# Performance work log

Hardware: AMD Instinct MI355X
Metric: run time of the kernel (lower is better)

## Reference

```python
import math
import jax, jax.numpy as jnp
import numpy as np

N_HEAD = 16
D_MODEL = 1024
D_K = 64
D_V = 64


def setup_inputs() -> dict:
    key = jax.random.key(0)
    ks = jax.random.split(key, 9)
    bs, s = 8, 1024
    q = jax.random.normal(ks[0], (bs, s, D_K), dtype=jnp.float32)
    k = jax.random.normal(ks[1], (bs, s, D_K), dtype=jnp.float32)
    v = jax.random.normal(ks[2], (bs, s, D_V), dtype=jnp.float32)
    # NOTE: the source module only ever uses linear_q (applied to q, k, v alike),
    # so we only materialize that projection. Torch Linear: y = x @ W.T + b.
    Wq = jax.random.normal(ks[3], (N_HEAD * D_K, D_K), dtype=jnp.float32) * 0.02
    bq = jnp.zeros((N_HEAD * D_K,), dtype=jnp.float32)
    W1 = jax.random.normal(ks[4], (D_MODEL, N_HEAD * D_V), dtype=jnp.float32) * 0.02
    b1 = jnp.zeros((D_MODEL,), dtype=jnp.float32)
    W2 = jax.random.normal(ks[5], (D_MODEL, D_MODEL), dtype=jnp.float32) * 0.02
    b2 = jnp.zeros((D_MODEL,), dtype=jnp.float32)
    return {"q": q, "k": k, "v": v, "Wq": Wq, "bq": bq,
            "W1": W1, "b1": b1, "W2": W2, "b2": b2}


def reference(q, k, v, Wq, bq, W1, b1, W2, b2):
    bs, s_q, d_k = q.shape
    h = N_HEAD
    scale = math.sqrt(d_k)
    # shared projection (source uses linear_q for all three); split heads on last dim
    proj = lambda x: (jnp.einsum('bsd,ed->bse', x, Wq) + bq).reshape(bs, -1, h, d_k)
    qh = proj(q)   # [b, s_q, h, d]
    kh = proj(k)   # [b, s_k, h, d]
    vh = proj(v)   # [b, s_v, h, d]
    e = jnp.einsum('bqhd,bkhd->bhqk', qh, kh) / scale
    a = jax.nn.softmax(e, axis=-1)  # dropout = identity in eval mode
    y = jnp.einsum('bhqk,bkhd->bqhd', a, vh).reshape(bs, s_q, h * d_k)
    # output MLP: Linear -> ReLU -> (dropout) -> Linear
    x = jax.nn.relu(jnp.einsum('bsd,ed->bse', y, W1) + b1)
    x = jnp.einsum('bsd,ed->bse', x, W2) + b2
    return x
```

## Files before the change

kernel.cpp:

```cpp
#include <hip/hip_runtime.h>
#include <math.h>

#define NB 8
#define SS 1024
#define NH 16
#define DK 64
#define EE 1024
#define DMOD 1024

using bf16x8 = __attribute__((ext_vector_type(8))) short;
using f32x4  = __attribute__((ext_vector_type(4))) float;

__device__ __forceinline__ unsigned short f2bf(float f) {
    unsigned u = __builtin_bit_cast(unsigned, f);
    u += 0x7FFFu + ((u >> 16) & 1u);
    return (unsigned short)(u >> 16);
}

__device__ __forceinline__ float exp2_hw(float x) {
#if __has_builtin(__builtin_amdgcn_exp2f)
    return __builtin_amdgcn_exp2f(x);
#else
    float r; asm("v_exp_f32 %0, %1" : "=v"(r) : "v"(x)); return r;
#endif
}

__device__ __forceinline__ unsigned cvt_pk_bf16(float lo, float hi) {
    unsigned r;
    asm("v_cvt_pk_bf16_f32 %0, %1, %2" : "=v"(r) : "v"(lo), "v"(hi));
    return r;
}

__device__ __forceinline__ void gld16(const void* g, void* l) {
    __builtin_amdgcn_global_load_lds(
        (const __attribute__((address_space(1))) void*)g,
        (__attribute__((address_space(3))) void*)l, 16, 0, 0);
}

__global__ __launch_bounds__(256) void cvt_all(
    const float* __restrict__ W1, const float* __restrict__ W2,
    const float* __restrict__ q, const float* __restrict__ k,
    const float* __restrict__ v, const float* __restrict__ Wq,
    unsigned short* __restrict__ W1b, unsigned short* __restrict__ W2b,
    unsigned short* __restrict__ qb, unsigned short* __restrict__ kb,
    unsigned short* __restrict__ vb, unsigned short* __restrict__ Wqb)
{
    const int z = blockIdx.y;
    const float* s; unsigned short* d; int n;
    switch (z) {
        case 0:  s = W1; d = W1b; n = 1048576; break;
        case 1:  s = W2; d = W2b; n = 1048576; break;
        case 2:  s = q;  d = qb;  n = 524288;  break;
        case 3:  s = k;  d = kb;  n = 524288;  break;
        case 4:  s = v;  d = vb;  n = 524288;  break;
        default: s = Wq; d = Wqb; n = 65536;   break;
    }
    const int i = (blockIdx.x * 256 + threadIdx.x) * 8;
    if (i >= n) return;
    const float4 a = *(const float4*)(s + i);
    const float4 b = *(const float4*)(s + i + 4);
    bf16x8 o;
    o[0]=(short)f2bf(a.x); o[1]=(short)f2bf(a.y); o[2]=(short)f2bf(a.z); o[3]=(short)f2bf(a.w);
    o[4]=(short)f2bf(b.x); o[5]=(short)f2bf(b.y); o[6]=(short)f2bf(b.z); o[7]=(short)f2bf(b.w);
    *(bf16x8*)(d + i) = o;
}

__global__ __launch_bounds__(256) void proj_mfma(
    const unsigned short* __restrict__ qb, const unsigned short* __restrict__ kb,
    const unsigned short* __restrict__ vb, const unsigned short* __restrict__ Wb,
    const float* __restrict__ bias, unsigned short* __restrict__ Cbase,
    float qscale)
{
    __shared__ __align__(16) unsigned short As[128 * 64];
    __shared__ __align__(16) unsigned short Bs[128 * 64];
    const int z = blockIdx.z;
    const unsigned short* X = (z == 0) ? qb : (z == 1) ? kb : vb;
    unsigned short* C = Cbase + (size_t)z * 8388608;
    const float sc = (z == 0) ? qscale : 1.0f;
    const int tid  = threadIdx.x;
    const int lane = tid & 63;
    const int w = tid >> 6, wm = w >> 1, wn = w & 1;
    const int n0 = blockIdx.x * 128, m0 = blockIdx.y * 128;
    const int lr = lane & 15, lg = lane >> 4;

    #pragma unroll
    for (int p = 0; p < 4; ++p) {
        const int c = p * 256 + tid;
        const int lb = (p * 256 + (tid & ~63)) * 8;
        gld16(X  + (size_t)m0 * DK + (size_t)c * 8, As + lb);
        gld16(Wb + (size_t)n0 * DK + (size_t)c * 8, Bs + lb);
    }
    __syncthreads();

    f32x4 acc[4][4] = {};
    #pragma unroll
    for (int kk = 0; kk < 2; ++kk) {
        bf16x8 af[4], bfr[4];
        #pragma unroll
        for (int mf = 0; mf < 4; ++mf)
            af[mf] = *(const bf16x8*)&As[(wm * 64 + mf * 16 + lr) * 64 + kk * 32 + lg * 8];
        #pragma unroll
        for (int nf = 0; nf < 4; ++nf)
            bfr[nf] = *(const bf16x8*)&Bs[(wn * 64 + nf * 16 + lr) * 64 + kk * 32 + lg * 8];
        #pragma unroll
        for (int mf = 0; mf < 4; ++mf)
            #pragma unroll
            for (int nf = 0; nf < 4; ++nf)
                acc[mf][nf] = __builtin_amdgcn_mfma_f32_16x16x32_bf16(
                    af[mf], bfr[nf], acc[mf][nf], 0, 0, 0);
    }

    #pragma unroll
    for (int nf = 0; nf < 4; ++nf) {
        const int n = n0 + wn * 64 + nf * 16 + lr;
        const float bb = bias[n];
        #pragma unroll
        for (int mf = 0; mf < 4; ++mf)
            #pragma unroll
            for (int r = 0; r < 4; ++r) {
                const int mr = m0 + wm * 64 + mf * 16 + lg * 4 + r;
                const int bh = (mr >> 10) * NH + (n >> 6);
                const int s  = mr & 1023, d = n & 63;
                const size_t idx = (z == 2)
                    ? (size_t)bh * 65536 + (size_t)d * 1024 + s
                    : (size_t)bh * 65536 + (size_t)s * 64 + d;
                C[idx] = f2bf((acc[mf][nf][r] + bb) * sc);
            }
    }
}

__global__ __launch_bounds__(256) void attn_v13(
    const unsigned short* __restrict__ Qp, const unsigned short* __restrict__ Kp,
    const unsigned short* __restrict__ Vt, unsigned short* __restrict__ Y)
{
    __shared__ __align__(16) unsigned short Ks[64 * 64];
    __shared__ __align__(16) unsigned short Vs[64 * 64];
    __shared__ __align__(16) unsigned short Ps[4][32][72];
    const int tid  = threadIdx.x;
    const int lane = tid & 63;
    const int w    = tid >> 6;
    const int flat    = blockIdx.x;
    const int logical = (flat & 7) * 128 + (flat >> 3);
    const int qt = logical & 7;
    const int bh = logical >> 3;
    const int q0 = qt * 128;
    const size_t base = (size_t)bh * (SS * DK);
    const int lr = lane & 15, lg = lane >> 4;
    const int lg4 = lg * 4;

    const int c0 = tid,       r0 = c0 >> 3, h0 = c0 & 7;
    const int c1 = 256 + tid, r1 = c1 >> 3, h1 = c1 & 7;
    const int lds0 = r0 * 64 + ((h0 ^ (r0 & 7)) << 3);
    const int lds1 = r1 * 64 + ((h1 ^ (r1 & 7)) << 3);

    const unsigned short* kbase = Kp + base;
    const unsigned short* vbase = Vt + base;
    bf16x8 kA = *(const bf16x8*)(kbase + (size_t)r0 * DK + h0 * 8);
    bf16x8 kB = *(const bf16x8*)(kbase + (size_t)r1 * DK + h1 * 8);
    bf16x8 vA = *(const bf16x8*)(vbase + (size_t)r0 * SS + h0 * 8);
    bf16x8 vB = *(const bf16x8*)(vbase + (size_t)r1 * SS + h1 * 8);
    *(bf16x8*)&Ks[lds0] = kA; *(bf16x8*)&Ks[lds1] = kB;
    *(bf16x8*)&Vs[lds0] = vA; *(bf16x8*)&Vs[lds1] = vB;

    bf16x8 bQ[2][2];
    #pragma unroll
    for (int qf = 0; qf < 2; ++qf) {
        const unsigned short* qptr =
            Qp + base + (size_t)(q0 + w * 32 + qf * 16 + lr) * DK + lg * 8;
        bQ[qf][0] = *(const bf16x8*)qptr;
        bQ[qf][1] = *(const bf16x8*)(qptr + 32);
    }

    __syncthreads();

    float lacc[2] = {0.0f, 0.0f};
    f32x4 oacc[2][4] = {};

    for (int kt = 0; kt < 16; ++kt) {
        if (kt < 15) {
            const int s1 = (kt + 1) * 64;
            kA = *(const bf16x8*)(kbase + (size_t)(s1 + r0) * DK + h0 * 8);
            kB = *(const bf16x8*)(kbase + (size_t)(s1 + r1) * DK + h1 * 8);
            vA = *(const bf16x8*)(vbase + (size_t)r0 * SS + s1 + h0 * 8);
            vB = *(const bf16x8*)(vbase + (size_t)r1 * SS + s1 + h1 * 8);
        }

        f32x4 sacc[2][4];
        #pragma unroll
        for (int nb = 0; nb < 4; ++nb) {
            const int krow = nb * 16 + lr;
            const bf16x8 aK0 = *(const bf16x8*)&Ks[krow * 64 + ((lg       ^ (lr & 7)) << 3)];
            const bf16x8 aK1 = *(const bf16x8*)&Ks[krow * 64 + (((4 + lg) ^ (lr & 7)) << 3)];
            #pragma unroll
            for (int qf = 0; qf < 2; ++qf) {
                f32x4 z = {};
                z = __builtin_amdgcn_mfma_f32_16x16x32_bf16(aK0, bQ[qf][0], z, 0, 0, 0);
                z = __builtin_amdgcn_mfma_f32_16x16x32_bf16(aK1, bQ[qf][1], z, 0, 0, 0);
                sacc[qf][nb] = z;
            }
        }

        bf16x8 bV[2][4];
        #pragma unroll
        for (int kk = 0; kk < 2; ++kk)
            #pragma unroll
            for (int d0 = 0; d0 < 4; ++d0) {
                const int vrow = d0 * 16 + lr;
                bV[kk][d0] = *(const bf16x8*)&Vs[vrow * 64 + (((kk * 4 + lg) ^ (lr & 7)) << 3)];
            }

        #pragma unroll
        for (int qf = 0; qf < 2; ++qf) {
            float p[4][4];
            float ls0 = 0.0f, ls1 = 0.0f;
            #pragma unroll
            for (int nb = 0; nb < 4; ++nb) {
                #pragma unroll
                for (int r = 0; r < 4; ++r) {
                    const float pv = exp2_hw(sacc[qf][nb][r]);
                    p[nb][r] = pv;
                    if (r & 1) ls1 += pv; else ls0 += pv;
                }
            }
            lacc[qf] += ls0 + ls1;

            #pragma unroll
            for (int nb = 0; nb < 4; ++nb) {
                uint2 pw;
                pw.x = cvt_pk_bf16(p[nb][0], p[nb][1]);
                pw.y = cvt_pk_bf16(p[nb][2], p[nb][3]);
                *(uint2*)&Ps[w][qf * 16 + lr][nb * 16 + lg4] = pw;
            }

            #pragma unroll
            for (int kk = 0; kk < 2; ++kk) {
                const bf16x8 aP = *(const bf16x8*)&Ps[w][qf * 16 + lr][kk * 32 + lg * 8];
                #pragma unroll
                for (int d0 = 0; d0 < 4; ++d0)
                    oacc[qf][d0] = __builtin_amdgcn_mfma_f32_16x16x32_bf16(
                        aP, bV[kk][d0], oacc[qf][d0], 0, 0, 0);
            }
        }

        if (kt < 15) {
            __syncthreads();
            *(bf16x8*)&Ks[lds0] = kA; *(bf16x8*)&Ks[lds1] = kB;
            *(bf16x8*)&Vs[lds0] = vA; *(bf16x8*)&Vs[lds1] = vB;
            __syncthreads();
        }
    }

    const int hh = bh & 15, bb = bh >> 4;
    #pragma unroll
    for (int qf = 0; qf < 2; ++qf) {
        float l = lacc[qf];
        l += __shfl_xor(l, 16);
        l += __shfl_xor(l, 32);
        const float linv = 1.0f / l;
        #pragma unroll
        for (int r = 0; r < 4; ++r) {
            const float lri = __shfl(linv, lg4 + r, 16);
            const int qr = q0 + w * 32 + qf * 16 + lg4 + r;
            unsigned short* dst = Y + (size_t)(bb * SS + qr) * EE + hh * DK;
            #pragma unroll
            for (int d0 = 0; d0 < 4; ++d0)
                dst[d0 * 16 + lr] = f2bf(oacc[qf][d0][r] * lri);
        }
    }
}

template<bool RELU, bool OUT_BF16>
__global__ __launch_bounds__(256) void mlp_gemm(
    const unsigned short* __restrict__ A, const unsigned short* __restrict__ B,
    const float* __restrict__ bias, void* __restrict__ Cv)
{
    constexpr int K = 1024, N = 1024;
    __shared__ __align__(16) unsigned short As[2][128 * 64];
    __shared__ __align__(16) unsigned short Bs[2][128 * 64];
    const int tid  = threadIdx.x;
    const int lane = tid & 63;
    const int w = tid >> 6, wm = w >> 1, wn = w & 1;
    const int flat    = blockIdx.x;
    const int logical = (flat & 7) * 64 + (flat >> 3);
    const int n0 = (logical & 7) * 128, m0 = (logical >> 3) * 128;
    const int lr = lane & 15, lg = lane >> 4;

    #pragma unroll
    for (int p = 0; p < 4; ++p) {
        const int c = p * 256 + tid;
        const int row = c >> 3, col = (c & 7) * 8;
        const int lb = (p * 256 + (tid & ~63)) * 8;
        gld16(A + (size_t)(m0 + row) * K + col, As[0] + lb);
        gld16(B + (size_t)(n0 + row) * K + col, Bs[0] + lb);
    }
    __syncthreads();

    f32x4 acc[4][4] = {};

    #pragma unroll
    for (int kt = 0; kt < 16; ++kt) {
        const int cur = kt & 1;
        if (kt < 15) {
            const int ko = (kt + 1) * 64;
            #pragma unroll
            for (int p = 0; p < 4; ++p) {
                const int c = p * 256 + tid;
                const int row = c >> 3, col = (c & 7) * 8;
                const int lb = (p * 256 + (tid & ~63)) * 8;
                gld16(A + (size_t)(m0 + row) * K + ko + col, As[cur ^ 1] + lb);
                gld16(B + (size_t)(n0 + row) * K + ko + col, Bs[cur ^ 1] + lb);
            }
        }
        #pragma unroll
        for (int kk = 0; kk < 2; ++kk) {
            bf16x8 af[4], bfr[4];
            #pragma unroll
            for (int mf = 0; mf < 4; ++mf)
                af[mf] = *(const bf16x8*)&As[cur][(wm * 64 + mf * 16 + lr) * 64 + kk * 32 + lg * 8];
            #pragma unroll
            for (int nf = 0; nf < 4; ++nf)
                bfr[nf] = *(const bf16x8*)&Bs[cur][(wn * 64 + nf * 16 + lr) * 64 + kk * 32 + lg * 8];
            #pragma unroll
            for (int mf = 0; mf < 4; ++mf)
                #pragma unroll
                for (int nf = 0; nf < 4; ++nf)
                    acc[mf][nf] = __builtin_amdgcn_mfma_f32_16x16x32_bf16(
                        af[mf], bfr[nf], acc[mf][nf], 0, 0, 0);
        }
        __syncthreads();
    }

    #pragma unroll
    for (int nf = 0; nf < 4; ++nf) {
        const int cc = n0 + wn * 64 + nf * 16 + lr;
        const float bb = bias[cc];
        #pragma unroll
        for (int mf = 0; mf < 4; ++mf) {
            #pragma unroll
            for (int r = 0; r < 4; ++r) {
                float x = acc[mf][nf][r] + bb;
                if (RELU) x = fmaxf(x, 0.0f);
                const size_t rr = (size_t)(m0 + wm * 64 + mf * 16 + lg * 4 + r);
                if (OUT_BF16) ((unsigned short*)Cv)[rr * N + cc] = f2bf(x);
                else          ((float*)Cv)[rr * N + cc] = x;
            }
        }
    }
}

extern "C" void kernel_launch(void* const* d_in, const int* in_sizes, int n_in,
                              void* d_out, int out_size, void* d_ws, size_t ws_size,
                              hipStream_t stream) {
    const float* q  = (const float*)d_in[0];
    const float* k  = (const float*)d_in[1];
    const float* v  = (const float*)d_in[2];
    const float* Wq = (const float*)d_in[3];
    const float* bq = (const float*)d_in[4];
    const float* W1 = (const float*)d_in[5];
    const float* b1 = (const float*)d_in[6];
    const float* W2 = (const float*)d_in[7];
    const float* b2 = (const float*)d_in[8];

    unsigned short* wsu = (unsigned short*)d_ws;
    unsigned short* Qp  = wsu;
    unsigned short* Kp  = wsu + (size_t)8388608;
    unsigned short* Vt  = wsu + (size_t)16777216;
    unsigned short* Y   = wsu + (size_t)25165824;
    unsigned short* W1b = wsu + (size_t)33554432;
    unsigned short* W2b = wsu + (size_t)34603008;
    unsigned short* qb  = wsu + (size_t)35651584;
    unsigned short* kb  = wsu + (size_t)36175872;
    unsigned short* vb  = wsu + (size_t)36700160;
    unsigned short* Wqb = wsu + (size_t)37224448;
    unsigned short* H1  = Qp;

    dim3 blk(256);

    cvt_all<<<dim3(512, 6), blk, 0, stream>>>(W1, W2, q, k, v, Wq,
                                              W1b, W2b, qb, kb, vb, Wqb);

    const float qscale = 0.125f * 1.44269504088896340736f;
    proj_mfma<<<dim3(8, 64, 3), blk, 0, stream>>>(qb, kb, vb, Wqb, bq, Qp, qscale);

    attn_v13<<<1024, blk, 0, stream>>>(Qp, Kp, Vt, Y);

    mlp_gemm<true,  true ><<<512, blk, 0, stream>>>(Y,  W1b, b1, H1);
    mlp_gemm<false, false><<<512, blk, 0, stream>>>(H1, W2b, b2, d_out);
}
```

Measured before the change: 135.3 us.

## Switch attention to 32x32x16 MFMA with register-resident P via permlane32 swap

Rewrites the attention kernel to use 32x32x16 bf16 MFMA tiles in place of 16x16x32. The S^T = K·Q^T accumulator layout lets the softmax probabilities be repacked in registers with v_permlane32_swap and fed directly as the A operand of the P·V MFMA. This removes the per-wave LDS staging buffer for P and its write/read round trip. The cost is larger accumulator register footprint, which could lower occupancy, and more complex output indexing and row-sum shuffles.

Result: no change. 133.8 us (-1.1%).

```diff
diff --git a/kernel.cpp b/kernel.cpp
--- a/kernel.cpp
+++ b/kernel.cpp
@@ -10,6 +10,7 @@
 
 using bf16x8 = __attribute__((ext_vector_type(8))) short;
 using f32x4  = __attribute__((ext_vector_type(4))) float;
+using f32x16 = __attribute__((ext_vector_type(16))) float;
 
 __device__ __forceinline__ unsigned short f2bf(float f) {
     unsigned u = __builtin_bit_cast(unsigned, f);
@@ -29,6 +30,10 @@
     unsigned r;
     asm("v_cvt_pk_bf16_f32 %0, %1, %2" : "=v"(r) : "v"(lo), "v"(hi));
     return r;
+}
+
+__device__ __forceinline__ void plane32_swap(unsigned& a, unsigned& b) {
+    asm volatile("v_permlane32_swap_b32 %0, %1" : "+v"(a), "+v"(b));
 }
 
 __device__ __forceinline__ void gld16(const void* g, void* l) {
@@ -129,13 +134,12 @@
     }
 }
 
-__global__ __launch_bounds__(256) void attn_v13(
+__global__ __launch_bounds__(256) void attn_v14(
     const unsigned short* __restrict__ Qp, const unsigned short* __restrict__ Kp,
     const unsigned short* __restrict__ Vt, unsigned short* __restrict__ Y)
 {
     __shared__ __align__(16) unsigned short Ks[64 * 64];
     __shared__ __align__(16) unsigned short Vs[64 * 64];
-    __shared__ __align__(16) unsigned short Ps[4][32][72];
     const int tid  = threadIdx.x;
     const int lane = tid & 63;
     const int w    = tid >> 6;
@@ -145,8 +149,8 @@
     const int bh = logical >> 3;
     const int q0 = qt * 128;
     const size_t base = (size_t)bh * (SS * DK);
-    const int lr = lane & 15, lg = lane >> 4;
-    const int lg4 = lg * 4;
+    const int q31 = lane & 31, hi = lane >> 5;
+    const int l7  = lane & 7;
 
     const int c0 = tid,       r0 = c0 >> 3, h0 = c0 & 7;
     const int c1 = 256 + tid, r1 = c1 >> 3, h1 = c1 & 7;
@@ -162,19 +166,18 @@
     *(bf16x8*)&Ks[lds0] = kA; *(bf16x8*)&Ks[lds1] = kB;
     *(bf16x8*)&Vs[lds0] = vA; *(bf16x8*)&Vs[lds1] = vB;
 
-    bf16x8 bQ[2][2];
-    #pragma unroll
-    for (int qf = 0; qf < 2; ++qf) {
-        const unsigned short* qptr =
-            Qp + base + (size_t)(q0 + w * 32 + qf * 16 + lr) * DK + lg * 8;
-        bQ[qf][0] = *(const bf16x8*)qptr;
-        bQ[qf][1] = *(const bf16x8*)(qptr + 32);
+    bf16x8 bQ[4];
+    {
+        const unsigned short* qptr = Qp + base + (size_t)(q0 + w * 32 + q31) * DK;
+        #pragma unroll
+        for (int ch = 0; ch < 4; ++ch)
+            bQ[ch] = *(const bf16x8*)(qptr + ch * 16 + hi * 8);
     }
 
     __syncthreads();
 
-    float lacc[2] = {0.0f, 0.0f};
-    f32x4 oacc[2][4] = {};
+    float lacc = 0.0f;
+    f32x16 oacc[2] = {};
 
     for (int kt = 0; kt < 16; ++kt) {
         if (kt < 15) {
@@ -185,60 +188,52 @@
             vB = *(const bf16x8*)(vbase + (size_t)r1 * SS + s1 + h1 * 8);
         }
 
-        f32x4 sacc[2][4];
-        #pragma unroll
-        for (int nb = 0; nb < 4; ++nb) {
-            const int krow = nb * 16 + lr;
-            const bf16x8 aK0 = *(const bf16x8*)&Ks[krow * 64 + ((lg       ^ (lr & 7)) << 3)];
-            const bf16x8 aK1 = *(const bf16x8*)&Ks[krow * 64 + (((4 + lg) ^ (lr & 7)) << 3)];
-            #pragma unroll
-            for (int qf = 0; qf < 2; ++qf) {
-                f32x4 z = {};
-                z = __builtin_amdgcn_mfma_f32_16x16x32_bf16(aK0, bQ[qf][0], z, 0, 0, 0);
-                z = __builtin_amdgcn_mfma_f32_16x16x32_bf16(aK1, bQ[qf][1], z, 0, 0, 0);
-                sacc[qf][nb] = z;
-            }
-        }
-
-        bf16x8 bV[2][4];
-        #pragma unroll
-        for (int kk = 0; kk < 2; ++kk)
-            #pragma unroll
-            for (int d0 = 0; d0 < 4; ++d0) {
-                const int vrow = d0 * 16 + lr;
-                bV[kk][d0] = *(const bf16x8*)&Vs[vrow * 64 + (((kk * 4 + lg) ^ (lr & 7)) << 3)];
-            }
-
-        #pragma unroll
-        for (int qf = 0; qf < 2; ++qf) {
-            float p[4][4];
-            float ls0 = 0.0f, ls1 = 0.0f;
-            #pragma unroll
-            for (int nb = 0; nb < 4; ++nb) {
-                #pragma unroll
-                for (int r = 0; r < 4; ++r) {
-                    const float pv = exp2_hw(sacc[qf][nb][r]);
-                    p[nb][r] = pv;
-                    if (r & 1) ls1 += pv; else ls0 += pv;
-                }
-            }
-            lacc[qf] += ls0 + ls1;
-
-            #pragma unroll
-            for (int nb = 0; nb < 4; ++nb) {
-                uint2 pw;
-                pw.x = cvt_pk_bf16(p[nb][0], p[nb][1]);
-                pw.y = cvt_pk_bf16(p[nb][2], p[nb][3]);
-                *(uint2*)&Ps[w][qf * 16 + lr][nb * 16 + lg4] = pw;
-            }
-
-            #pragma unroll
-            for (int kk = 0; kk < 2; ++kk) {
-                const bf16x8 aP = *(const bf16x8*)&Ps[w][qf * 16 + lr][kk * 32 + lg * 8];
-                #pragma unroll
-                for (int d0 = 0; d0 < 4; ++d0)
-                    oacc[qf][d0] = __builtin_amdgcn_mfma_f32_16x16x32_bf16(
-                        aP, bV[kk][d0], oacc[qf][d0], 0, 0, 0);
+        f32x16 sacc[2];
+        #pragma unroll
+        for (int kb = 0; kb < 2; ++kb) {
+            f32x16 z = {};
+            #pragma unroll
+            for (int ch = 0; ch < 4; ++ch) {
+                const int row = kb * 32 + q31;
+                const bf16x8 aK = *(const bf16x8*)&Ks[row * 64 + (((2 * ch + hi) ^ l7) << 3)];
+                z = __builtin_amdgcn_mfma_f32_32x32x16_bf16(aK, bQ[ch], z, 0, 0, 0);
+            }
+            sacc[kb] = z;
+        }
+
+        bf16x8 pa[2][2];
+        #pragma unroll
+        for (int kb = 0; kb < 2; ++kb) {
+            float p[16];
+            float ls = 0.0f;
+            #pragma unroll
+            for (int r = 0; r < 16; ++r) {
+                p[r] = exp2_hw(sacc[kb][r]);
+                ls += p[r];
+            }
+            lacc += ls;
+            unsigned D[8];
+            #pragma unroll
+            for (int u = 0; u < 8; ++u)
+                D[u] = cvt_pk_bf16(p[2 * u], p[2 * u + 1]);
+            plane32_swap(D[0], D[2]);
+            plane32_swap(D[1], D[3]);
+            plane32_swap(D[4], D[6]);
+            plane32_swap(D[5], D[7]);
+            uint4 w0; w0.x = D[0]; w0.y = D[1]; w0.z = D[2]; w0.w = D[3];
+            uint4 w1; w1.x = D[4]; w1.y = D[5]; w1.z = D[6]; w1.w = D[7];
+            pa[kb][0] = __builtin_bit_cast(bf16x8, w0);
+            pa[kb][1] = __builtin_bit_cast(bf16x8, w1);
+        }
+
+        #pragma unroll
+        for (int db = 0; db < 2; ++db) {
+            #pragma unroll
+            for (int c = 0; c < 4; ++c) {
+                const int row = db * 32 + q31;
+                const bf16x8 bV = *(const bf16x8*)&Vs[row * 64 + (((2 * c + hi) ^ l7) << 3)];
+                oacc[db] = __builtin_amdgcn_mfma_f32_32x32x16_bf16(
+                    pa[c >> 1][c & 1], bV, oacc[db], 0, 0, 0);
             }
         }
 
@@ -251,21 +246,17 @@
     }
 
     const int hh = bh & 15, bb = bh >> 4;
-    #pragma unroll
-    for (int qf = 0; qf < 2; ++qf) {
-        float l = lacc[qf];
-        l += __shfl_xor(l, 16);
-        l += __shfl_xor(l, 32);
-        const float linv = 1.0f / l;
-        #pragma unroll
-        for (int r = 0; r < 4; ++r) {
-            const float lri = __shfl(linv, lg4 + r, 16);
-            const int qr = q0 + w * 32 + qf * 16 + lg4 + r;
-            unsigned short* dst = Y + (size_t)(bb * SS + qr) * EE + hh * DK;
-            #pragma unroll
-            for (int d0 = 0; d0 < 4; ++d0)
-                dst[d0 * 16 + lr] = f2bf(oacc[qf][d0][r] * lri);
-        }
+    float l = lacc;
+    l += __shfl_xor(l, 32);
+    const float linv = 1.0f / l;
+    #pragma unroll
+    for (int r = 0; r < 16; ++r) {
+        const int qrl = (r & 3) + 8 * (r >> 2) + 4 * hi;
+        const float lri = __shfl(linv, qrl, 32);
+        const int qr = q0 + w * 32 + qrl;
+        unsigned short* dst = Y + (size_t)(bb * SS + qr) * EE + hh * DK + q31;
+        dst[0]  = f2bf(oacc[0][r] * lri);
+        dst[32] = f2bf(oacc[1][r] * lri);
     }
 }
 
@@ -382,7 +373,7 @@
     const float qscale = 0.125f * 1.44269504088896340736f;
     proj_mfma<<<dim3(8, 64, 3), blk, 0, stream>>>(qb, kb, vb, Wqb, bq, Qp, qscale);
 
-    attn_v13<<<1024, blk, 0, stream>>>(Qp, Kp, Vt, Y);
+    attn_v14<<<1024, blk, 0, stream>>>(Qp, Kp, Vt, Y);
 
     mlp_gemm<true,  true ><<<512, blk, 0, stream>>>(Y,  W1b, b1, H1);
     mlp_gemm<false, false><<<512, blk, 0, stream>>>(H1, W2b, b2, d_out);
```
